# Optimization experiments

Measured on AMD Instinct MI355X. Metric: run time of the kernel, lower is better.

## Reference

```python
import jax, jax.numpy as jnp
import numpy as np

B = 8192          # batch size (positions)
FPP = 32          # active features per position (NNUE: 32 pieces)
NNZ = B * FPP     # 262144
FT_OUT = 1024
N_FEAT = 49152
N_VFEAT = 768


def setup_inputs() -> dict:
    key = jax.random.key(0)
    ks = jax.random.split(key, 6)
    stm_feat = jax.random.randint(ks[0], (NNZ,), 0, N_FEAT, dtype=jnp.int32)
    nstm_feat = jax.random.randint(ks[1], (NNZ,), 0, N_FEAT, dtype=jnp.int32)
    batch_idx = jnp.repeat(jnp.arange(B, dtype=jnp.int32), FPP)  # exactly FPP feats per sample
    values = jnp.ones((NNZ,), jnp.float32)
    s = 0.02
    W_ft = jax.random.normal(ks[2], (N_FEAT, FT_OUT), jnp.float32) * s   # Linear weight, pre-transposed [in, out]
    b_ft = jax.random.normal(ks[3], (FT_OUT,), jnp.float32) * s
    W_fft = jax.random.normal(ks[4], (N_VFEAT, FT_OUT), jnp.float32) * s
    b_fft = jnp.zeros((FT_OUT,), jnp.float32)
    W_out = jax.random.normal(ks[5], (2 * FT_OUT, 1), jnp.float32) * s
    b_out = jnp.zeros((1,), jnp.float32)
    return {
        "values": values, "stm_feat": stm_feat, "nstm_feat": nstm_feat,
        "batch_idx": batch_idx, "W_ft": W_ft, "b_ft": b_ft,
        "W_fft": W_fft, "b_fft": b_fft, "W_out": W_out, "b_out": b_out,
        "size": B,
    }


def reference(values, stm_feat, nstm_feat, batch_idx, W_ft, b_ft, W_fft, b_fft, W_out, b_out, size):
    # sparse @ W.T + b  ==  per-sample gather-sum of weight rows (embedding-bag) + bias
    def side_ft(feat):
        vw = values[:, None]                                   # [nnz,1]
        g = jax.ops.segment_sum(W_ft[feat] * vw, batch_idx, num_segments=size)        # [B, FT_OUT]
        gv = jax.ops.segment_sum(W_fft[feat % N_VFEAT] * vw, batch_idx, num_segments=size)
        return g + gv + b_ft + b_fft

    stm_ft = side_ft(stm_feat)
    nstm_ft = side_ft(nstm_feat)
    hidden = jnp.clip(jnp.concatenate([stm_ft, nstm_ft], axis=1), 0.0, 1.0)  # [B, 2*FT_OUT]
    return jax.nn.sigmoid(hidden @ W_out + b_out)                            # [B, 1]
```

## Files before the change

kernel.cpp:

```cpp
#include <hip/hip_runtime.h>

#define BATCH   8192
#define FPP     32
#define FT_OUT  1024
#define N_VFEAT 768
#define N_FEAT  49152

#define WQ_BYTES   ((size_t)N_FEAT * FT_OUT)
#define WS_NEEDED  (WQ_BYTES + (size_t)N_FEAT * 4)

typedef signed char c16 __attribute__((ext_vector_type(16)));
typedef float       f4  __attribute__((ext_vector_type(4)));

__global__ __launch_bounds__(256) void build_combined_i8(
    const float* __restrict__ W_ft,
    const float* __restrict__ W_fft,
    signed char* __restrict__ Wq,
    float*       __restrict__ scales)
{
    const int wave = threadIdx.x >> 6;
    const int lane = threadIdx.x & 63;
    const int f    = blockIdx.x * 4 + wave;
    const int fm   = (blockIdx.x % (N_VFEAT / 4)) * 4 + wave;

    const float* a = W_ft  + (size_t)f  * FT_OUT;
    const float* g = W_fft + (size_t)fm * FT_OUT;

    float c[16];
#pragma unroll
    for (int ch = 0; ch < 4; ++ch) {
        const f4 av = __builtin_nontemporal_load(
            reinterpret_cast<const f4*>(a + ch * 256 + lane * 4));
        const f4 gv = *reinterpret_cast<const f4*>(g + ch * 256 + lane * 4);
        c[ch * 4 + 0] = av.x + gv.x;
        c[ch * 4 + 1] = av.y + gv.y;
        c[ch * 4 + 2] = av.z + gv.z;
        c[ch * 4 + 3] = av.w + gv.w;
    }

    float m = 0.0f;
#pragma unroll
    for (int j = 0; j < 16; ++j) m = fmaxf(m, fabsf(c[j]));
#pragma unroll
    for (int o = 32; o > 0; o >>= 1)
        m = fmaxf(m, __shfl_xor(m, o, 64));

    const float am  = fmaxf(m, 1e-20f);
    const float inv = 127.0f / am;
    if (lane == 0) scales[f] = am / 127.0f;

#pragma unroll
    for (int ch = 0; ch < 4; ++ch) {
        int q0 = (int)rintf(c[ch * 4 + 0] * inv);
        int q1 = (int)rintf(c[ch * 4 + 1] * inv);
        int q2 = (int)rintf(c[ch * 4 + 2] * inv);
        int q3 = (int)rintf(c[ch * 4 + 3] * inv);
        q0 = max(-127, min(127, q0));
        q1 = max(-127, min(127, q1));
        q2 = max(-127, min(127, q2));
        q3 = max(-127, min(127, q3));
        char4 pk;
        pk.x = (signed char)q0; pk.y = (signed char)q1;
        pk.z = (signed char)q2; pk.w = (signed char)q3;
        *reinterpret_cast<char4*>(Wq + (size_t)f * FT_OUT + ch * 256 + lane * 4) = pk;
    }
}

__global__ __launch_bounds__(256) void nnue_fwd_i8(
    const float*       __restrict__ values,
    const int*         __restrict__ stm_feat,
    const int*         __restrict__ nstm_feat,
    const signed char* __restrict__ Wq,
    const float*       __restrict__ scales,
    const float*       __restrict__ b_ft,
    const float*       __restrict__ b_fft,
    const float*       __restrict__ W_out,
    const float*       __restrict__ b_out,
    float*             __restrict__ out)
{
    const int tid  = threadIdx.x;
    const int wave = tid >> 6;
    const int lane = tid & 63;
    const int bl   = wave >> 1;
    const int sd   = wave & 1;
    const int c0   = lane * 16;

    __shared__ int   s_off[2][2][FPP];
    __shared__ float s_vs [2][2][FPP];
    __shared__ float s_red[2][2];

    if (tid < 128) {
        const int lb = tid >> 6;
        const int ls = (tid >> 5) & 1;
        const int k  = tid & 31;
        const int b  = blockIdx.x * 2 + lb;
        const int f  = (ls ? nstm_feat : stm_feat)[b * FPP + k];
        s_off[lb][ls][k] = f * FT_OUT;
        s_vs [lb][ls][k] = values[b * FPP + k] * scales[f];
    }
    __syncthreads();

    float acc[16];
#pragma unroll
    for (int j = 0; j < 16; ++j) acc[j] = 0.0f;

#pragma unroll 8
    for (int k = 0; k < FPP; ++k) {
        const c16 q = *reinterpret_cast<const c16*>(Wq + s_off[bl][sd][k] + c0);
        const float vs = s_vs[bl][sd][k];
#pragma unroll
        for (int j = 0; j < 16; ++j)
            acc[j] += vs * (float)q[j];
    }

    float partial = 0.0f;
#pragma unroll
    for (int ch = 0; ch < 4; ++ch) {
        const float4 bf = *reinterpret_cast<const float4*>(b_ft  + c0 + 4 * ch);
        const float4 bg = *reinterpret_cast<const float4*>(b_fft + c0 + 4 * ch);
        const float4 wo = *reinterpret_cast<const float4*>(W_out + sd * FT_OUT + c0 + 4 * ch);
        float h;
        h = acc[ch * 4 + 0] + bf.x + bg.x; h = fminf(fmaxf(h, 0.0f), 1.0f); partial += h * wo.x;
        h = acc[ch * 4 + 1] + bf.y + bg.y; h = fminf(fmaxf(h, 0.0f), 1.0f); partial += h * wo.y;
        h = acc[ch * 4 + 2] + bf.z + bg.z; h = fminf(fmaxf(h, 0.0f), 1.0f); partial += h * wo.z;
        h = acc[ch * 4 + 3] + bf.w + bg.w; h = fminf(fmaxf(h, 0.0f), 1.0f); partial += h * wo.w;
    }

#pragma unroll
    for (int o = 32; o > 0; o >>= 1)
        partial += __shfl_down(partial, o, 64);

    if (lane == 0) s_red[bl][sd] = partial;
    __syncthreads();

    if (tid < 2) {
        float x = s_red[tid][0] + s_red[tid][1] + b_out[0];
        out[blockIdx.x * 2 + tid] = 1.0f / (1.0f + __expf(-x));
    }
}

__global__ __launch_bounds__(256) void nnue_fwd_f32(
    const float* __restrict__ values,
    const int*   __restrict__ stm_feat,
    const int*   __restrict__ nstm_feat,
    const float* __restrict__ W_ft,
    const float* __restrict__ b_ft,
    const float* __restrict__ W_fft,
    const float* __restrict__ b_fft,
    const float* __restrict__ W_out,
    const float* __restrict__ b_out,
    float*       __restrict__ out)
{
    const int b    = blockIdx.x;
    const int tid  = threadIdx.x;
    const int side = tid >> 7;
    const int lane = tid & 127;
    const int c0   = lane * 8;

    __shared__ int   s_off_ft [2][FPP];
    __shared__ int   s_off_fft[2][FPP];
    __shared__ float s_val[FPP];
    __shared__ float s_red[4];

    if (tid < FPP) {
        int f = stm_feat[b * FPP + tid];
        s_off_ft [0][tid] = f * FT_OUT;
        s_off_fft[0][tid] = (f % N_VFEAT) * FT_OUT;
        s_val[tid] = values[b * FPP + tid];
    } else if (tid < 2 * FPP) {
        int k = tid - FPP;
        int f = nstm_feat[b * FPP + k];
        s_off_ft [1][k] = f * FT_OUT;
        s_off_fft[1][k] = (f % N_VFEAT) * FT_OUT;
    }
    __syncthreads();

    float acc[8];
#pragma unroll
    for (int j = 0; j < 8; ++j) acc[j] = 0.0f;

#pragma unroll 4
    for (int k = 0; k < FPP; ++k) {
        const float* ra = W_ft  + s_off_ft [side][k] + c0;
        const float* rg = W_fft + s_off_fft[side][k] + c0;
        const float4 a0 = *reinterpret_cast<const float4*>(ra);
        const float4 a1 = *reinterpret_cast<const float4*>(ra + 4);
        const float4 g0 = *reinterpret_cast<const float4*>(rg);
        const float4 g1 = *reinterpret_cast<const float4*>(rg + 4);
        const float v = s_val[k];
        acc[0] += (a0.x + g0.x) * v;  acc[1] += (a0.y + g0.y) * v;
        acc[2] += (a0.z + g0.z) * v;  acc[3] += (a0.w + g0.w) * v;
        acc[4] += (a1.x + g1.x) * v;  acc[5] += (a1.y + g1.y) * v;
        acc[6] += (a1.z + g1.z) * v;  acc[7] += (a1.w + g1.w) * v;
    }

    float partial = 0.0f;
#pragma unroll
    for (int j = 0; j < 8; ++j) {
        float h = acc[j] + b_ft[c0 + j] + b_fft[c0 + j];
        h = fminf(fmaxf(h, 0.0f), 1.0f);
        partial += h * W_out[side * FT_OUT + c0 + j];
    }
#pragma unroll
    for (int o = 32; o > 0; o >>= 1)
        partial += __shfl_down(partial, o, 64);
    const int wv = tid >> 6;
    if ((tid & 63) == 0) s_red[wv] = partial;
    __syncthreads();
    if (tid == 0) {
        float x = s_red[0] + s_red[1] + s_red[2] + s_red[3] + b_out[0];
        out[b] = 1.0f / (1.0f + __expf(-x));
    }
}

extern "C" void kernel_launch(void* const* d_in, const int* in_sizes, int n_in,
                              void* d_out, int out_size, void* d_ws, size_t ws_size,
                              hipStream_t stream) {
    const float* values    = (const float*)d_in[0];
    const int*   stm_feat  = (const int*)d_in[1];
    const int*   nstm_feat = (const int*)d_in[2];
    const float* W_ft      = (const float*)d_in[4];
    const float* b_ft      = (const float*)d_in[5];
    const float* W_fft     = (const float*)d_in[6];
    const float* b_fft     = (const float*)d_in[7];
    const float* W_out     = (const float*)d_in[8];
    const float* b_out     = (const float*)d_in[9];
    float*       out       = (float*)d_out;

    if (ws_size >= WS_NEEDED) {
        signed char* Wq     = (signed char*)d_ws;
        float*       scales = (float*)((char*)d_ws + WQ_BYTES);

        build_combined_i8<<<N_FEAT / 4, 256, 0, stream>>>(W_ft, W_fft, Wq, scales);

        nnue_fwd_i8<<<BATCH / 2, 256, 0, stream>>>(
            values, stm_feat, nstm_feat, Wq, scales, b_ft, b_fft, W_out, b_out, out);
    } else {
        nnue_fwd_f32<<<BATCH, 256, 0, stream>>>(
            values, stm_feat, nstm_feat, W_ft, b_ft, W_fft, b_fft, W_out, b_out, out);
    }
}
```

Before: 359.1 us.

## Accumulate gathered int8 rows with packed int16 dot2 instead of float FMAs

Stores quantized weights as offset-binary uint8 and quantizes the per-feature value*scale coefficients to int16 per sample. The gather loop then pairs two features and uses v_dot2_i32_i16 with byte permutes to accumulate in integers, and a per-sample sum term corrects for the 128 offset afterward. The intent is to replace int8-to-float conversions and FMAs in the inner loop with fewer integer dot instructions. This adds a second quantization step that costs precision, plus extra shuffles in the setup phase.

```diff
diff --git a/kernel.cpp b/kernel.cpp
--- a/kernel.cpp
+++ b/kernel.cpp
@@ -9,13 +9,23 @@
 #define WQ_BYTES   ((size_t)N_FEAT * FT_OUT)
 #define WS_NEEDED  (WQ_BYTES + (size_t)N_FEAT * 4)
 
-typedef signed char c16 __attribute__((ext_vector_type(16)));
-typedef float       f4  __attribute__((ext_vector_type(4)));
+typedef float f4 __attribute__((ext_vector_type(4)));
+typedef short s2 __attribute__((ext_vector_type(2)));
+
+static __device__ __forceinline__ int sdot2(int a, int b, int c) {
+#if __has_builtin(__builtin_amdgcn_sdot2)
+    return __builtin_amdgcn_sdot2(__builtin_bit_cast(s2, a), __builtin_bit_cast(s2, b), c, false);
+#else
+    int d;
+    asm volatile("v_dot2_i32_i16 %0, %1, %2, %3" : "=v"(d) : "v"(a), "v"(b), "v"(c));
+    return d;
+#endif
+}
 
 __global__ __launch_bounds__(256) void build_combined_i8(
     const float* __restrict__ W_ft,
     const float* __restrict__ W_fft,
-    signed char* __restrict__ Wq,
+    unsigned char* __restrict__ Wq,
     float*       __restrict__ scales)
 {
     const int wave = threadIdx.x >> 6;
@@ -55,28 +65,28 @@
         int q1 = (int)rintf(c[ch * 4 + 1] * inv);
         int q2 = (int)rintf(c[ch * 4 + 2] * inv);
         int q3 = (int)rintf(c[ch * 4 + 3] * inv);
-        q0 = max(-127, min(127, q0));
-        q1 = max(-127, min(127, q1));
-        q2 = max(-127, min(127, q2));
-        q3 = max(-127, min(127, q3));
-        char4 pk;
-        pk.x = (signed char)q0; pk.y = (signed char)q1;
-        pk.z = (signed char)q2; pk.w = (signed char)q3;
-        *reinterpret_cast<char4*>(Wq + (size_t)f * FT_OUT + ch * 256 + lane * 4) = pk;
+        q0 = max(-127, min(127, q0)) + 128;
+        q1 = max(-127, min(127, q1)) + 128;
+        q2 = max(-127, min(127, q2)) + 128;
+        q3 = max(-127, min(127, q3)) + 128;
+        uchar4 pk;
+        pk.x = (unsigned char)q0; pk.y = (unsigned char)q1;
+        pk.z = (unsigned char)q2; pk.w = (unsigned char)q3;
+        *reinterpret_cast<uchar4*>(Wq + (size_t)f * FT_OUT + ch * 256 + lane * 4) = pk;
     }
 }
 
 __global__ __launch_bounds__(256) void nnue_fwd_i8(
-    const float*       __restrict__ values,
-    const int*         __restrict__ stm_feat,
-    const int*         __restrict__ nstm_feat,
-    const signed char* __restrict__ Wq,
-    const float*       __restrict__ scales,
-    const float*       __restrict__ b_ft,
-    const float*       __restrict__ b_fft,
-    const float*       __restrict__ W_out,
-    const float*       __restrict__ b_out,
-    float*             __restrict__ out)
+    const float*         __restrict__ values,
+    const int*           __restrict__ stm_feat,
+    const int*           __restrict__ nstm_feat,
+    const unsigned char* __restrict__ Wq,
+    const float*         __restrict__ scales,
+    const float*         __restrict__ b_ft,
+    const float*         __restrict__ b_fft,
+    const float*         __restrict__ W_out,
+    const float*         __restrict__ b_out,
+    float*               __restrict__ out)
 {
     const int tid  = threadIdx.x;
     const int wave = tid >> 6;
@@ -85,33 +95,68 @@
     const int sd   = wave & 1;
     const int c0   = lane * 16;
 
-    __shared__ int   s_off[2][2][FPP];
-    __shared__ float s_vs [2][2][FPP];
-    __shared__ float s_red[2][2];
+    __shared__ int   s_off [2][2][FPP];
+    __shared__ int   s_tp  [2][2][FPP / 2];
+    __shared__ float s_sig [2][2];
+    __shared__ int   s_tsum[2][2];
+    __shared__ float s_red [2][2];
 
     if (tid < 128) {
-        const int lb = tid >> 6;
-        const int ls = (tid >> 5) & 1;
+        const int g  = tid >> 5;
+        const int lb = g >> 1;
+        const int ls = g & 1;
         const int k  = tid & 31;
         const int b  = blockIdx.x * 2 + lb;
         const int f  = (ls ? nstm_feat : stm_feat)[b * FPP + k];
         s_off[lb][ls][k] = f * FT_OUT;
-        s_vs [lb][ls][k] = values[b * FPP + k] * scales[f];
-    }
-    __syncthreads();
-
-    float acc[16];
-#pragma unroll
-    for (int j = 0; j < 16; ++j) acc[j] = 0.0f;
-
-#pragma unroll 8
-    for (int k = 0; k < FPP; ++k) {
-        const c16 q = *reinterpret_cast<const c16*>(Wq + s_off[bl][sd][k] + c0);
-        const float vs = s_vs[bl][sd][k];
-#pragma unroll
-        for (int j = 0; j < 16; ++j)
-            acc[j] += vs * (float)q[j];
-    }
+        const float vs = values[b * FPP + k] * scales[f];
+
+        float vmax = fabsf(vs);
+#pragma unroll
+        for (int o = 16; o > 0; o >>= 1)
+            vmax = fmaxf(vmax, __shfl_xor(vmax, o, 32));
+        vmax = fmaxf(vmax, 1e-30f);
+
+        const int t = (int)rintf(vs * (32767.0f / vmax));
+        int tsum = t;
+#pragma unroll
+        for (int o = 16; o > 0; o >>= 1)
+            tsum += __shfl_xor(tsum, o, 32);
+        const int tnext = __shfl_down(t, 1, 32);
+        if ((k & 1) == 0)
+            s_tp[lb][ls][k >> 1] = (t & 0xffff) | (tnext << 16);
+        if (k == 0) {
+            s_sig [lb][ls] = vmax / 32767.0f;
+            s_tsum[lb][ls] = tsum;
+        }
+    }
+    __syncthreads();
+
+    int acci[16];
+#pragma unroll
+    for (int j = 0; j < 16; ++j) acci[j] = 0;
+
+#define DOT_STEP(d, av, bv)                                                          \
+    acci[4*(d)+0] = sdot2(tp, (int)__builtin_amdgcn_perm((av), (bv), 0x0C000C04u), acci[4*(d)+0]); \
+    acci[4*(d)+1] = sdot2(tp, (int)__builtin_amdgcn_perm((av), (bv), 0x0C010C05u), acci[4*(d)+1]); \
+    acci[4*(d)+2] = sdot2(tp, (int)__builtin_amdgcn_perm((av), (bv), 0x0C020C06u), acci[4*(d)+2]); \
+    acci[4*(d)+3] = sdot2(tp, (int)__builtin_amdgcn_perm((av), (bv), 0x0C030C07u), acci[4*(d)+3]);
+
+#pragma unroll 4
+    for (int kp = 0; kp < FPP / 2; ++kp) {
+        const uint4 qa = *reinterpret_cast<const uint4*>(Wq + s_off[bl][sd][2 * kp]     + c0);
+        const uint4 qb = *reinterpret_cast<const uint4*>(Wq + s_off[bl][sd][2 * kp + 1] + c0);
+        const int tp = s_tp[bl][sd][kp];
+        DOT_STEP(0, qa.x, qb.x)
+        DOT_STEP(1, qa.y, qb.y)
+        DOT_STEP(2, qa.z, qb.z)
+        DOT_STEP(3, qa.w, qb.w)
+    }
+#undef DOT_STEP
+
+    const float sigma = s_sig [bl][sd];
+    const int   tsum  = s_tsum[bl][sd];
+    const int   corr  = 128 * tsum;
 
     float partial = 0.0f;
 #pragma unroll
@@ -120,10 +165,14 @@
         const float4 bg = *reinterpret_cast<const float4*>(b_fft + c0 + 4 * ch);
         const float4 wo = *reinterpret_cast<const float4*>(W_out + sd * FT_OUT + c0 + 4 * ch);
         float h;
-        h = acc[ch * 4 + 0] + bf.x + bg.x; h = fminf(fmaxf(h, 0.0f), 1.0f); partial += h * wo.x;
-        h = acc[ch * 4 + 1] + bf.y + bg.y; h = fminf(fmaxf(h, 0.0f), 1.0f); partial += h * wo.y;
-        h = acc[ch * 4 + 2] + bf.z + bg.z; h = fminf(fmaxf(h, 0.0f), 1.0f); partial += h * wo.z;
-        h = acc[ch * 4 + 3] + bf.w + bg.w; h = fminf(fmaxf(h, 0.0f), 1.0f); partial += h * wo.w;
+        h = sigma * (float)(acci[ch * 4 + 0] - corr) + bf.x + bg.x;
+        h = fminf(fmaxf(h, 0.0f), 1.0f); partial += h * wo.x;
+        h = sigma * (float)(acci[ch * 4 + 1] - corr) + bf.y + bg.y;
+        h = fminf(fmaxf(h, 0.0f), 1.0f); partial += h * wo.y;
+        h = sigma * (float)(acci[ch * 4 + 2] - corr) + bf.z + bg.z;
+        h = fminf(fmaxf(h, 0.0f), 1.0f); partial += h * wo.z;
+        h = sigma * (float)(acci[ch * 4 + 3] - corr) + bf.w + bg.w;
+        h = fminf(fmaxf(h, 0.0f), 1.0f); partial += h * wo.w;
     }
 
 #pragma unroll
@@ -228,8 +277,8 @@
     float*       out       = (float*)d_out;
 
     if (ws_size >= WS_NEEDED) {
-        signed char* Wq     = (signed char*)d_ws;
-        float*       scales = (float*)((char*)d_ws + WQ_BYTES);
+        unsigned char* Wq     = (unsigned char*)d_ws;
+        float*         scales = (float*)((char*)d_ws + WQ_BYTES);
 
         build_combined_i8<<<N_FEAT / 4, 256, 0, stream>>>(W_ft, W_fft, Wq, scales);
 
```

New measurement: 358.6 us. Within noise of the previous version (-0.1%).
